# Kernel tuning notes

Measured on AMD Instinct MI355X. Metric: run time of the kernel, lower is better.

## Reference

```python
import jax, jax.numpy as jnp
import numpy as np

B, S, D, H = 2, 2048, 1024, 4
DK = D // H


def setup_inputs() -> dict:
    key = jax.random.key(0)
    ks = jax.random.split(key, 12)
    inp = {
        "Q_input": jax.random.normal(ks[0], (B, S, D), jnp.float32),
        "K": jax.random.normal(ks[1], (B, S, D), jnp.float32),
        "V": jax.random.normal(ks[2], (B, S, D), jnp.float32),
        "T_field": jax.random.normal(ks[3], (32, 32, 16, 16), jnp.float32),
        "Wq_w": jax.random.normal(ks[4], (D, D), jnp.float32) * 0.02,
        "Wq_b": jnp.zeros((D,), jnp.float32),
        "Wo_w": jax.random.normal(ks[5], (D, D), jnp.float32) * 0.02,
        "Wo_b": jnp.zeros((D,), jnp.float32),
        "proj_w": jax.random.normal(ks[6], (24, DK), jnp.float32) * 0.02,
        "proj_b": jnp.zeros((24,), jnp.float32),
        "geo_w": jnp.ones((4,), jnp.float32),
        "temperature": jnp.asarray(1.0, jnp.float32),
    }
    return inp


def _psi(x, proj_w, proj_b):
    # x: (B,H,S,DK) -> 16D real biquaternion via (A,B,Theta) -> A*exp(Th)+B*exp(i*Th)
    gen = x @ proj_w.T + proj_b                      # (B,H,S,24)
    A, Bg = gen[..., 0:8], gen[..., 8:16]
    Th = jnp.clip(gen[..., 16:24], -8.0, 8.0)
    psi_real = A * jnp.exp(Th) + Bg * jnp.cos(Th)
    psi_imag = Bg * jnp.sin(Th)
    return jnp.concatenate([psi_real, psi_imag], axis=-1)  # (B,H,S,16)


def reference(Q_input, K, V, T_field, Wq_w, Wq_b, Wo_w, Wo_b, proj_w, proj_b, geo_w, temperature):
    b, sq, d = Q_input.shape
    sk = K.shape[1]
    dk = d // H
    Q = (Q_input @ Wq_w.T + Wq_b).reshape(b, sq, H, dk).transpose(0, 2, 1, 3)
    Kh = K.reshape(b, sk, H, dk).transpose(0, 2, 1, 3)
    Vh = V.reshape(b, sk, H, dk).transpose(0, 2, 1, 3)
    pq = _psi(Q, proj_w, proj_b)   # (b,H,sq,16)
    pk = _psi(Kh, proj_w, proj_b)  # (b,H,sk,16)
    qr, qi = pq[..., :8], pq[..., 8:]
    kr, ki = pk[..., :8], pk[..., 8:]
    # tensor: real part of complex inner product; spinor: imaginary (rotational) part
    tensor = jnp.einsum('bhqd,bhkd->bhqk', qr, kr) + jnp.einsum('bhqd,bhkd->bhqk', qi, ki)
    spinor = jnp.einsum('bhqd,bhkd->bhqk', qr, ki) - jnp.einsum('bhqd,bhkd->bhqk', qi, kr)
    qn2 = jnp.sum(pq * pq, -1)  # (b,H,sq)
    kn2 = jnp.sum(pk * pk, -1)  # (b,H,sk)
    gram = qn2[..., :, None] * kn2[..., None, :]
    # wedge: antisymmetric span magnitude (Gram residual)
    wedge = jnp.sqrt(jnp.maximum(gram - tensor**2 - spinor**2, 0.0) + 1e-6)
    # hodge: amplitude contraction (rank-2 -> rank-1 conservation)
    hodge = jnp.sqrt(qn2 + 1e-6)[..., :, None] * jnp.sqrt(kn2 + 1e-6)[..., None, :]
    scores = (geo_w[0] * wedge + geo_w[1] * tensor + geo_w[2] * spinor + geo_w[3] * hodge) / 4.0
    scores = scores / temperature
    w = jax.nn.softmax(scores, axis=-1)              # dropout disabled (eval)
    out = jnp.einsum('bhqk,bhkd->bhqd', w, Vh)
    out = out.transpose(0, 2, 1, 3).reshape(b, sq, d)
    return out @ Wo_w.T + Wo_b
```

## Files before the change

### kernel.cpp

```cpp
#include <hip/hip_runtime.h>
#include <hip/hip_bf16.h>
#include <math.h>

#define B_ 2
#define S_ 2048
#define D_ 1024
#define H_ 4
#define DK_ 256
#define NJ 24
#define NG 96
#define KTA 128
#define NT2 (S_ / KTA)

typedef _Float16 f16;
typedef _Float16 f16x2 __attribute__((ext_vector_type(2)));
typedef _Float16 f16x4 __attribute__((ext_vector_type(4)));
typedef _Float16 f16x8 __attribute__((ext_vector_type(8)));
typedef float f32x16 __attribute__((ext_vector_type(16)));
typedef float v2f __attribute__((ext_vector_type(2)));

__global__ __launch_bounds__(256) void k_prep(
    const float* __restrict__ Wq_w, const float* __restrict__ proj_w,
    const float* __restrict__ Wq_b, const float* __restrict__ proj_b,
    const float* __restrict__ Wo_w, const float* __restrict__ V,
    f16* __restrict__ Mf, f16* __restrict__ Mkf,
    float* __restrict__ cbias, float* __restrict__ pbias,
    f16* __restrict__ Wf, f16* __restrict__ Vt2, float* __restrict__ khm) {
  __shared__ f16 tile[64][72];
  const int bid = blockIdx.x;
  const int t = threadIdx.x;
  if (bid < 384) {
    int tid = bid * 256 + t;
    int hj = tid >> 10, d = tid & 1023;
    int h = hj / NJ, j = hj - h * NJ;
    const float* wq = Wq_w + (size_t)(h * DK_) * D_ + d;
    const float* pw = proj_w + j * DK_;
    float acc = 0.f;
#pragma unroll 8
    for (int k = 0; k < DK_; ++k) acc += wq[(size_t)k * D_] * pw[k];
    Mf[(size_t)hj * D_ + d] = (f16)acc;
  } else if (bid == 384) {
    if (t < NG) {
      int h = t / NJ, j = t - h * NJ;
      float acc = proj_b[j];
      for (int k = 0; k < DK_; ++k) acc += Wq_b[h * DK_ + k] * proj_w[j * DK_ + k];
      cbias[t] = acc;
      pbias[t] = proj_b[j];
    }
    if (t < 8) ((unsigned int*)khm)[t] = 0u;
  } else if (bid < 769) {
    int tid = (bid - 385) * 256 + t;
    int hj = tid >> 10, d = tid & 1023;
    int h = hj / NJ, j = hj - h * NJ;
    float v = ((d >> 8) == h) ? proj_w[j * DK_ + (d & 255)] : 0.f;
    Mkf[tid] = (f16)v;
  } else if (bid < 1281) {
    int i = ((bid - 769) * 256 + t) * 8;
    float4 a = *(const float4*)(Wo_w + i);
    float4 b = *(const float4*)(Wo_w + i + 4);
    f16x8 o = {(f16)a.x, (f16)a.y, (f16)a.z, (f16)a.w,
               (f16)b.x, (f16)b.y, (f16)b.z, (f16)b.w};
    *(f16x8*)(Wf + i) = o;
  } else {
    int vbid = bid - 1281;
    int s0 = (vbid & 31) * 64, c0 = ((vbid >> 5) & 3) * 64;
    int bh = vbid >> 7;
    int b = bh >> 2, h = bh & 3;
    const float* src = V + (size_t)b * S_ * D_ + h * DK_ + c0;
#pragma unroll
    for (int u = 0; u < 4; ++u) {
      int row = (t >> 4) + 16 * u;
      int c4 = (t & 15) * 4;
      float4 v = *(const float4*)(src + (size_t)(s0 + row) * D_ + c4);
      tile[c4 + 0][row] = (f16)v.x;
      tile[c4 + 1][row] = (f16)v.y;
      tile[c4 + 2][row] = (f16)v.z;
      tile[c4 + 3][row] = (f16)v.w;
    }
    __syncthreads();
#pragma unroll
    for (int u = 0; u < 2; ++u) {
      int sid = t + 256 * u;
      int sgroup = sid & 7, dkl = sid >> 3;
      int dk = c0 + dkl, s = s0 + sgroup * 8;
      int wv = dk >> 5, qq = dk & 31;
      int kt = s >> 7, ks = (s >> 4) & 7, lhh = (s >> 3) & 1;
      size_t idx = ((((size_t)(bh * 8 + wv) * 16 + kt) * 8 + ks) * 2 + lhh) * 256 + qq * 8;
      *(f16x8*)(Vt2 + idx) = *(const f16x8*)&tile[dkl][sgroup * 8];
    }
  }
}

__global__ __launch_bounds__(256, 1) void k_gen(
    const float* __restrict__ Q, const float* __restrict__ Kin,
    const f16* __restrict__ Mf, const f16* __restrict__ Mkf,
    const float* __restrict__ cbias, const float* __restrict__ pbias,
    f16* __restrict__ pqF, float* __restrict__ qn2,
    f16* __restrict__ pkF, float* __restrict__ kn2,
    float* __restrict__ khm) {
  __shared__ __align__(16) f16 Xs[8192];
  __shared__ __align__(16) f16 Bs[24576];
  __shared__ __align__(16) float redP[4][32][96];
  __shared__ float genL[32][100];

  const int t = threadIdx.x;
  const int w = t >> 6, lane = t & 63;
  const int l31 = lane & 31, lh = lane >> 5;
  const bool isQ = blockIdx.x < 128;
  const int r0 = (isQ ? blockIdx.x : blockIdx.x - 128) * 32;
  const float* X = isQ ? Q : Kin;
  const f16* Bf = isQ ? Mf : Mkf;
  const float* bias = isQ ? cbias : pbias;

  int xrow[8], xk4[8];
#pragma unroll
  for (int u = 0; u < 8; ++u) {
    int idx = t + 256 * u;
    xrow[u] = idx >> 6;
    xk4[u] = idx & 63;
  }
  int bcol[12], bkg[12];
#pragma unroll
  for (int u = 0; u < 12; ++u) {
    int idx = t + 256 * u;
    bcol[u] = idx >> 5;
    bkg[u] = idx & 31;
  }

  float4 xr[8];
  f16x8 br[12];
#define XLOAD(K0)                                                              \
  {                                                                            \
    _Pragma("unroll") for (int u = 0; u < 8; ++u) xr[u] =                      \
        *(const float4*)(X + (size_t)(r0 + xrow[u]) * D_ + (K0) + xk4[u] * 4); \
  }
#define BLOAD(K0)                                                            \
  {                                                                          \
    _Pragma("unroll") for (int u = 0; u < 12; ++u) br[u] =                   \
        *(const f16x8*)(Bf + (size_t)bcol[u] * D_ + (K0) + bkg[u] * 8);      \
  }
#define XWRITE()                                                            \
  {                                                                         \
    _Pragma("unroll") for (int u = 0; u < 8; ++u) {                         \
      f16x4 v = {(f16)xr[u].x, (f16)xr[u].y, (f16)xr[u].z, (f16)xr[u].w};   \
      *(f16x4*)&Xs[((xk4[u] >> 1) * 32 + xrow[u]) * 8 + (xk4[u] & 1) * 4] = v; \
    }                                                                       \
  }
#define BWRITE()                                                            \
  {                                                                         \
    _Pragma("unroll") for (int u = 0; u < 12; ++u)                          \
        *(f16x8*)&Bs[(bcol[u] >> 5) * 8192 + bkg[u] * 256 +                 \
                     (bcol[u] & 31) * 8] = br[u];                           \
  }

  XLOAD(0);
  BLOAD(0);
  XWRITE();
  BWRITE();
  __syncthreads();

  f32x16 acc0{}, acc1{}, acc2{};
  for (int ch = 0; ch < 4; ++ch) {
    if (ch < 3) {
      XLOAD((ch + 1) * 256);
      BLOAD((ch + 1) * 256);
    }
#pragma unroll
    for (int i = 0; i < 4; ++i) {
      const int kk = w * 4 + i;
      const int off = (kk * 2 + lh) * 256 + l31 * 8;
      f16x8 af = *(const f16x8*)&Xs[off];
      f16x8 b0 = *(const f16x8*)&Bs[off];
      f16x8 b1 = *(const f16x8*)&Bs[8192 + off];
      f16x8 b2 = *(const f16x8*)&Bs[16384 + off];
      acc0 = __builtin_amdgcn_mfma_f32_32x32x16_f16(af, b0, acc0, 0, 0, 0);
      acc1 = __builtin_amdgcn_mfma_f32_32x32x16_f16(af, b1, acc1, 0, 0, 0);
      acc2 = __builtin_amdgcn_mfma_f32_32x32x16_f16(af, b2, acc2, 0, 0, 0);
    }
    __syncthreads();
    if (ch < 3) {
      XWRITE();
      BWRITE();
      __syncthreads();
    }
  }
#undef XLOAD
#undef BLOAD
#undef XWRITE
#undef BWRITE

#pragma unroll
  for (int r = 0; r < 16; ++r) {
    const int row = (r & 3) + 8 * (r >> 2) + 4 * lh;
    redP[w][row][l31] = acc0[r];
    redP[w][row][32 + l31] = acc1[r];
    redP[w][row][64 + l31] = acc2[r];
  }
  __syncthreads();

  {
    const int row = t >> 3, cg = t & 7;
#pragma unroll
    for (int c = 0; c < 12; ++c) {
      int col = cg * 12 + c;
      genL[row][col] = redP[0][row][col] + redP[1][row][col] +
                       redP[2][row][col] + redP[3][row][col] + bias[col];
    }
  }
  __syncthreads();

  {
    const int rg = t >> 6;
    const int hh = (t & 63) >> 4;
    const int ii = t & 15;
    const int j = ii & 7;
    f16* po = isQ ? pqF : pkF;
    float* n2o = isQ ? qn2 : kn2;
    float mx = 0.f;
#pragma unroll 2
    for (int r = 0; r < 8; ++r) {
      int row = rg * 8 + r;
      int g = r0 + row;
      int b = g >> 11, s = g & (S_ - 1);
      const float* gl = &genL[row][hh * NJ];
      float A = gl[j], Bg = gl[8 + j];
      float Th = fminf(fmaxf(gl[16 + j], -8.f), 8.f);
      float val = (ii < 8) ? (A * __expf(Th) + Bg * __cosf(Th)) : (Bg * __sinf(Th));
      size_t base = (size_t)(b * H_ + hh) * S_ + s;
      po[base * 16 + ii] = (f16)val;
      float sq = val * val;
#pragma unroll
      for (int off = 1; off < 16; off <<= 1) sq += __shfl_xor(sq, off);
      if (ii == 0) {
        n2o[base] = sq;
        mx = fmaxf(mx, sq);
      }
    }
    if (!isQ && ii == 0) {
      int g = r0;
      int b = g >> 11;
      atomicMax((unsigned int*)&khm[b * H_ + hh], __float_as_uint(mx));
    }
  }
}

__global__ __launch_bounds__(512, 4) void k_attn(
    const f16* __restrict__ pqF, const float* __restrict__ qn2,
    const f16* __restrict__ pkF, const float* __restrict__ kn2,
    const f16* __restrict__ Vt2, const float* __restrict__ geo_w,
    const float* __restrict__ temp, const float* __restrict__ khm,
    f16* __restrict__ attnF) {
  __shared__ __align__(16) float kn2s[2][KTA];
  __shared__ __align__(16) float khs[2][KTA];
  __shared__ float sPart[8][32];
  __shared__ float linvL[32];
  __shared__ __align__(16) f16 Plds[2][16][32][8];

  const int t = threadIdx.x;
  const int w = t >> 6;
  const int lane = t & 63;
  const int q_ = lane & 31;
  const int lh = lane >> 5;

  const int bid = blockIdx.x;
  const int bh = bid & 7, qt = bid >> 3;
  const int q0 = qt * 32;
  const int b = bh >> 2, h = bh & 3;

  const size_t bhS = (size_t)bh * S_;
  const f16* pkb = pkF + bhS * 16;
  const float* kn2b = kn2 + bhS;

  const float scale = 0.25f / temp[0] * 1.4426950408889634f;
  const float g0s = geo_w[0] * scale, g1s = geo_w[1] * scale, g2s = geo_w[2] * scale;
  const float g3s = geo_w[3] * scale;

  const f16x8 bq = *(const f16x8*)(pqF + (bhS + q0 + q_) * 16 + lh * 8);
  const float qn2q = qn2[bhS + q0 + q_];
  const float qh = sqrtf(qn2q + 1e-6f);
  const float qh3 = qh * g3s;
  const float sumg = fabsf(g0s) + fabsf(g1s) + fabsf(g2s) + fabsf(g3s);
  const float Mhat = sumg * qh * sqrtf(khm[bh] + 1e-6f) - 4.328085123f;

  const v2f qn2v = {qn2q, qn2q};
  const v2f g0v = {g0s, g0s}, g1v = {g1s, g1s}, g2v = {g2s, g2s};
  const v2f zero2 = {0.f, 0.f}, eps2 = {1e-6f, 1e-6f};
  const v2f mhv = {Mhat, Mhat};

  const f16* ap_base = pkb + (size_t)(w * 16 + (q_ & 15)) * 16 +
                       ((q_ < 16) ? lh * 8 : (1 - lh) * 8);
  const f16* vb_lane = Vt2 + (size_t)(bh * 8 + w) * 16 * 4096 + lh * 256 + q_ * 8;

  if (t < KTA) {
    float kv = kn2b[t];
    kn2s[0][t] = kv;
    khs[0][t] = __builtin_amdgcn_sqrtf(kv + 1e-6f);
  }
  float lreg = 0.f;
  f32x16 acc{};
  const f32x16 zacc{};

  f16x8 af = *(const f16x8*)ap_base;
  f16x8 bv[8];
#pragma unroll
  for (int ks = 0; ks < 8; ++ks) bv[ks] = *(const f16x8*)(vb_lane + ks * 512);
  __syncthreads();

  for (int ktl = 0; ktl < NT2; ++ktl) {
    const int k0l = ktl * KTA;
    const int cb = ktl & 1, nb = cb ^ 1;

    float knv = 0.f;
    if (t < KTA && ktl + 1 < NT2) knv = kn2b[k0l + KTA + t];

    f16x8 afx = af;
    if (q_ >= 16 && lh == 1) afx = -afx;
    __builtin_amdgcn_s_setprio(1);
    f32x16 sc = __builtin_amdgcn_mfma_f32_32x32x16_f16(afx, bq, zacc, 0, 0, 0);
    __builtin_amdgcn_s_setprio(0);
    if (ktl + 1 < NT2) af = *(const f16x8*)(ap_base + (size_t)(k0l + KTA) * 16);

    float pv[8];
    v2f psv = {0.f, 0.f};
#pragma unroll
    for (int rp = 0; rp < 4; ++rp) {
      const int r = 2 * rp;
      const int kb2 = w * 16 + 4 * lh + (rp & 1) * 2 + (rp >> 1) * 8;
      v2f tn = {sc[r], sc[r + 1]};
      v2f sp = {sc[r + 8], sc[r + 9]};
      v2f kn2p = *(const v2f*)&kn2s[cb][kb2];
      v2f khp = *(const v2f*)&khs[cb][kb2];
      v2f wr = qn2v * kn2p - tn * tn - sp * sp;
      wr = __builtin_elementwise_max(wr, zero2) + eps2;
      v2f wg = {__builtin_amdgcn_sqrtf(wr.x), __builtin_amdgcn_sqrtf(wr.y)};
      v2f sv2 = g0v * wg + g1v * tn + g2v * sp + qh3 * khp - mhv;
      v2f p2 = {__builtin_amdgcn_exp2f(sv2.x), __builtin_amdgcn_exp2f(sv2.y)};
      pv[r] = p2.x;
      pv[r + 1] = p2.y;
      psv += p2;
    }
    lreg += psv.x + psv.y;

    if (t < KTA && ktl + 1 < NT2) {
      kn2s[nb][t] = knv;
      khs[nb][t] = __builtin_amdgcn_sqrtf(knv + 1e-6f);
    }
    {
      f16x2 p01 = {(f16)pv[0], (f16)pv[1]};
      f16x2 p23 = {(f16)pv[2], (f16)pv[3]};
      f16x2 p45 = {(f16)pv[4], (f16)pv[5]};
      f16x2 p67 = {(f16)pv[6], (f16)pv[7]};
      *(f16x2*)&Plds[cb][2 * w + 0][q_][4 * lh + 0] = p01;
      *(f16x2*)&Plds[cb][2 * w + 0][q_][4 * lh + 2] = p23;
      *(f16x2*)&Plds[cb][2 * w + 1][q_][4 * lh + 0] = p45;
      *(f16x2*)&Plds[cb][2 * w + 1][q_][4 * lh + 2] = p67;
    }
    __syncthreads();

    __builtin_amdgcn_s_setprio(1);
#pragma unroll
    for (int ks = 0; ks < 8; ++ks) {
      f16x8 pa = *(const f16x8*)&Plds[cb][2 * ks + lh][q_][0];
      acc = __builtin_amdgcn_mfma_f32_32x32x16_f16(pa, bv[ks], acc, 0, 0, 0);
    }
    __builtin_amdgcn_s_setprio(0);
    if (ktl + 1 < NT2) {
      const f16* vbn = vb_lane + (size_t)(ktl + 1) * 4096;
#pragma unroll
      for (int ks = 0; ks < 8; ++ks) bv[ks] = *(const f16x8*)(vbn + ks * 512);
    }
  }

  lreg += __shfl_xor(lreg, 32);
  if (lh == 0) sPart[w][q_] = lreg;
  __syncthreads();
  if (t < 32) {
    float s8 = 0.f;
#pragma unroll
    for (int i = 0; i < 8; ++i) s8 += sPart[i][t];
    linvL[t] = 1.f / s8;
  }
  __syncthreads();
  const size_t obase = ((size_t)b * S_ + q0) * D_ + h * DK_ + w * 32 + q_;
#pragma unroll
  for (int r = 0; r < 16; ++r) {
    const int row = (r & 3) + 8 * (r >> 2) + 4 * lh;
    attnF[obase + (size_t)row * D_] = (f16)(acc[r] * linvL[row]);
  }
}

__global__ __launch_bounds__(256, 1) void k_wo(const f16* __restrict__ A,
                                               const f16* __restrict__ Wt,
                                               const float* __restrict__ bias,
                                               float* __restrict__ C) {
  __shared__ __align__(16) f16 Abuf[2][128 * 64];
  __shared__ __align__(16) f16 Bbuf[2][128 * 64];
  const int t = threadIdx.x;
  const int w = t >> 6, lane = t & 63;
  const int wr = w >> 1, wc = w & 1;
  const int brow = blockIdx.y * 128, bcol = blockIdx.x * 128;

  int srow[4], skof[4];
#pragma unroll
  for (int u = 0; u < 4; ++u) {
    int c = t + 256 * u;
    int sub = c >> 6, l6 = c & 63;
    srow[u] = (sub >> 2) * 32 + (l6 & 31);
    skof[u] = (sub & 3) * 16 + (l6 >> 5) * 8;
  }

  uint4 ra0, ra1, ra2, ra3, rb0, rb1, rb2, rb3;
#define LOAD_TILE(K0)                                                        \
  {                                                                          \
    ra0 = *(const uint4*)(A + (size_t)(brow + srow[0]) * D_ + (K0) + skof[0]); \
    ra1 = *(const uint4*)(A + (size_t)(brow + srow[1]) * D_ + (K0) + skof[1]); \
    ra2 = *(const uint4*)(A + (size_t)(brow + srow[2]) * D_ + (K0) + skof[2]); \
    ra3 = *(const uint4*)(A + (size_t)(brow + srow[3]) * D_ + (K0) + skof[3]); \
    rb0 = *(const uint4*)(Wt + (size_t)(bcol + srow[0]) * D_ + (K0) + skof[0]); \
    rb1 = *(const uint4*)(Wt + (size_t)(bcol + srow[1]) * D_ + (K0) + skof[1]); \
    rb2 = *(const uint4*)(Wt + (size_t)(bcol + srow[2]) * D_ + (K0) + skof[2]); \
    rb3 = *(const uint4*)(Wt + (size_t)(bcol + srow[3]) * D_ + (K0) + skof[3]); \
  }
#define WRITE_TILE(BUF)                                       \
  {                                                           \
    *(uint4*)&Abuf[BUF][(t + 0) * 8] = ra0;                   \
    *(uint4*)&Abuf[BUF][(t + 256) * 8] = ra1;                 \
    *(uint4*)&Abuf[BUF][(t + 512) * 8] = ra2;                 \
    *(uint4*)&Abuf[BUF][(t + 768) * 8] = ra3;                 \
    *(uint4*)&Bbuf[BUF][(t + 0) * 8] = rb0;                   \
    *(uint4*)&Bbuf[BUF][(t + 256) * 8] = rb1;                 \
    *(uint4*)&Bbuf[BUF][(t + 512) * 8] = rb2;                 \
    *(uint4*)&Bbuf[BUF][(t + 768) * 8] = rb3;                 \
  }

  f32x16 acc00{}, acc01{}, acc10{}, acc11{};

  LOAD_TILE(0);
  WRITE_TILE(0);
  LOAD_TILE(64);
  __syncthreads();

  int cur = 0;
  for (int kt = 0; kt < 16; ++kt) {
    const int am0 = (wr * 2 + 0) * 4, am1 = (wr * 2 + 1) * 4;
    const int bn0 = (wc * 2 + 0) * 4, bn1 = (wc * 2 + 1) * 4;
#pragma unroll
    for (int kk = 0; kk < 4; ++kk) {
      f16x8 a0 = *(const f16x8*)&Abuf[cur][(am0 + kk) * 512 + lane * 8];
      f16x8 a1 = *(const f16x8*)&Abuf[cur][(am1 + kk) * 512 + lane * 8];
      f16x8 b0 = *(const f16x8*)&Bbuf[cur][(bn0 + kk) * 512 + lane * 8];
      f16x8 b1 = *(const f16x8*)&Bbuf[cur][(bn1 + kk) * 512 + lane * 8];
      acc00 = __builtin_amdgcn_mfma_f32_32x32x16_f16(a0, b0, acc00, 0, 0, 0);
      acc01 = __builtin_amdgcn_mfma_f32_32x32x16_f16(a0, b1, acc01, 0, 0, 0);
      acc10 = __builtin_amdgcn_mfma_f32_32x32x16_f16(a1, b0, acc10, 0, 0, 0);
      acc11 = __builtin_amdgcn_mfma_f32_32x32x16_f16(a1, b1, acc11, 0, 0, 0);
    }
    if (kt + 1 < 16) {
      WRITE_TILE(cur ^ 1);
      if (kt + 2 < 16) LOAD_TILE((kt + 2) * 64);
    }
    __syncthreads();
    cur ^= 1;
  }

  const int l31 = lane & 31, lh = lane >> 5;
  const float bv0 = bias[bcol + (wc * 2 + 0) * 32 + l31];
  const float bv1 = bias[bcol + (wc * 2 + 1) * 32 + l31];
#pragma unroll
  for (int r = 0; r < 16; ++r) {
    const int row = (r & 3) + 8 * (r >> 2) + 4 * lh;
    const size_t m0r = (size_t)(brow + (wr * 2 + 0) * 32 + row) * D_;
    const size_t m1r = (size_t)(brow + (wr * 2 + 1) * 32 + row) * D_;
    C[m0r + bcol + (wc * 2 + 0) * 32 + l31] = acc00[r] + bv0;
    C[m0r + bcol + (wc * 2 + 1) * 32 + l31] = acc01[r] + bv1;
    C[m1r + bcol + (wc * 2 + 0) * 32 + l31] = acc10[r] + bv0;
    C[m1r + bcol + (wc * 2 + 1) * 32 + l31] = acc11[r] + bv1;
  }
#undef LOAD_TILE
#undef WRITE_TILE
}

extern "C" void kernel_launch(void* const* d_in, const int* in_sizes, int n_in,
                              void* d_out, int out_size, void* d_ws, size_t ws_size,
                              hipStream_t stream) {
  const float* Q_input = (const float*)d_in[0];
  const float* K = (const float*)d_in[1];
  const float* V = (const float*)d_in[2];
  const float* Wq_w = (const float*)d_in[4];
  const float* Wq_b = (const float*)d_in[5];
  const float* Wo_w = (const float*)d_in[6];
  const float* Wo_b = (const float*)d_in[7];
  const float* proj_w = (const float*)d_in[8];
  const float* proj_b = (const float*)d_in[9];
  const float* geo_w = (const float*)d_in[10];
  const float* temp = (const float*)d_in[11];

  float* ws = (float*)d_ws;
  float* cbias = ws;
  float* pbias = cbias + 128;
  float* khm = pbias + 128;
  f16* Mf = (f16*)(khm + 128);
  f16* Mkf = Mf + 98304;
  float* qn2 = (float*)(Mkf + 98304);
  float* kn2 = qn2 + 16384;
  f16* pqF = (f16*)(kn2 + 16384);
  f16* pkF = pqF + 262144;
  f16* Vt2 = pkF + 262144;
  f16* attnF = Vt2 + 4194304;
  f16* Wf = attnF + 4194304;
  float* out = (float*)d_out;

  k_prep<<<dim3(2305), dim3(256), 0, stream>>>(Wq_w, proj_w, Wq_b, proj_b, Wo_w,
                                               V, Mf, Mkf, cbias, pbias, Wf, Vt2,
                                               khm);
  k_gen<<<dim3(256), dim3(256), 0, stream>>>(Q_input, K, Mf, Mkf, cbias, pbias,
                                             pqF, qn2, pkF, kn2, khm);
  k_attn<<<dim3(512), dim3(512), 0, stream>>>(pqF, qn2, pkF, kn2, Vt2, geo_w,
                                              temp, khm, attnF);
  k_wo<<<dim3(8, 32), dim3(256), 0, stream>>>(attnF, Wf, Wo_b, out);
}
```

Measured before the change: 103.0 us.

## Double attention key tile to 256 per iteration, halving barriers

The attention loop now processes 256 keys per iteration instead of 128. Each wave issues two score MFMAs and two sets of softmax exponentials, and sixteen PV MFMAs per step, with the shared score buffer and norm buffers doubled. The intent is to halve the per-tile barrier and loop overhead and expose more independent MFMA work. The cost is higher register and LDS use, and launch bounds are relaxed from four to two blocks per CU, which lowers occupancy.

```diff
diff --git a/kernel.cpp b/kernel.cpp
--- a/kernel.cpp
+++ b/kernel.cpp
@@ -9,8 +9,8 @@
 #define DK_ 256
 #define NJ 24
 #define NG 96
-#define KTA 128
-#define NT2 (S_ / KTA)
+#define KT2 256
+#define NT256 (S_ / KT2)
 
 typedef _Float16 f16;
 typedef _Float16 f16x2 __attribute__((ext_vector_type(2)));
@@ -244,17 +244,17 @@
   }
 }
 
-__global__ __launch_bounds__(512, 4) void k_attn(
+__global__ __launch_bounds__(512, 2) void k_attn(
     const f16* __restrict__ pqF, const float* __restrict__ qn2,
     const f16* __restrict__ pkF, const float* __restrict__ kn2,
     const f16* __restrict__ Vt2, const float* __restrict__ geo_w,
     const float* __restrict__ temp, const float* __restrict__ khm,
     f16* __restrict__ attnF) {
-  __shared__ __align__(16) float kn2s[2][KTA];
-  __shared__ __align__(16) float khs[2][KTA];
+  __shared__ __align__(16) float kn2s[2][KT2];
+  __shared__ __align__(16) float khs[2][KT2];
   __shared__ float sPart[8][32];
   __shared__ float linvL[32];
-  __shared__ __align__(16) f16 Plds[2][16][32][8];
+  __shared__ __align__(16) f16 Plds[2][32][32][8];
 
   const int t = threadIdx.x;
   const int w = t >> 6;
@@ -287,11 +287,11 @@
   const v2f zero2 = {0.f, 0.f}, eps2 = {1e-6f, 1e-6f};
   const v2f mhv = {Mhat, Mhat};
 
-  const f16* ap_base = pkb + (size_t)(w * 16 + (q_ & 15)) * 16 +
+  const f16* ap_base = pkb + (size_t)(w * 32 + (q_ & 15)) * 16 +
                        ((q_ < 16) ? lh * 8 : (1 - lh) * 8);
-  const f16* vb_lane = Vt2 + (size_t)(bh * 8 + w) * 16 * 4096 + lh * 256 + q_ * 8;
-
-  if (t < KTA) {
+  const f16* vt_base = Vt2 + (size_t)(bh * 8 + w) * 16 * 4096 + lh * 256 + q_ * 8;
+
+  if (t < KT2) {
     float kv = kn2b[t];
     kn2s[0][t] = kv;
     khs[0][t] = __builtin_amdgcn_sqrtf(kv + 1e-6f);
@@ -300,34 +300,40 @@
   f32x16 acc{};
   const f32x16 zacc{};
 
-  f16x8 af = *(const f16x8*)ap_base;
-  f16x8 bv[8];
-#pragma unroll
-  for (int ks = 0; ks < 8; ++ks) bv[ks] = *(const f16x8*)(vb_lane + ks * 512);
-  __syncthreads();
-
-  for (int ktl = 0; ktl < NT2; ++ktl) {
-    const int k0l = ktl * KTA;
+  f16x8 af0 = *(const f16x8*)ap_base;
+  f16x8 af1 = *(const f16x8*)(ap_base + 256);
+  f16x8 bv[8], bvB[8];
+#pragma unroll
+  for (int ks = 0; ks < 8; ++ks) bv[ks] = *(const f16x8*)(vt_base + ks * 512);
+#pragma unroll
+  for (int ks = 0; ks < 8; ++ks) bvB[ks] = *(const f16x8*)(vt_base + 4096 + ks * 512);
+  __syncthreads();
+
+  for (int ktl = 0; ktl < NT256; ++ktl) {
     const int cb = ktl & 1, nb = cb ^ 1;
 
     float knv = 0.f;
-    if (t < KTA && ktl + 1 < NT2) knv = kn2b[k0l + KTA + t];
-
-    f16x8 afx = af;
-    if (q_ >= 16 && lh == 1) afx = -afx;
+    if (t < KT2 && ktl + 1 < NT256) knv = kn2b[ktl * KT2 + KT2 + t];
+
+    f16x8 a0 = af0, a1 = af1;
+    if (q_ >= 16 && lh == 1) { a0 = -a0; a1 = -a1; }
     __builtin_amdgcn_s_setprio(1);
-    f32x16 sc = __builtin_amdgcn_mfma_f32_32x32x16_f16(afx, bq, zacc, 0, 0, 0);
+    f32x16 sc0 = __builtin_amdgcn_mfma_f32_32x32x16_f16(a0, bq, zacc, 0, 0, 0);
+    f32x16 sc1 = __builtin_amdgcn_mfma_f32_32x32x16_f16(a1, bq, zacc, 0, 0, 0);
     __builtin_amdgcn_s_setprio(0);
-    if (ktl + 1 < NT2) af = *(const f16x8*)(ap_base + (size_t)(k0l + KTA) * 16);
-
-    float pv[8];
+    if (ktl + 1 < NT256) {
+      af0 = *(const f16x8*)(ap_base + (size_t)(ktl + 1) * 4096);
+      af1 = *(const f16x8*)(ap_base + (size_t)(ktl + 1) * 4096 + 256);
+    }
+
+    float pv0[8], pv1[8];
     v2f psv = {0.f, 0.f};
 #pragma unroll
     for (int rp = 0; rp < 4; ++rp) {
       const int r = 2 * rp;
-      const int kb2 = w * 16 + 4 * lh + (rp & 1) * 2 + (rp >> 1) * 8;
-      v2f tn = {sc[r], sc[r + 1]};
-      v2f sp = {sc[r + 8], sc[r + 9]};
+      const int kb2 = w * 32 + 4 * lh + (rp & 1) * 2 + (rp >> 1) * 8;
+      v2f tn = {sc0[r], sc0[r + 1]};
+      v2f sp = {sc0[r + 8], sc0[r + 9]};
       v2f kn2p = *(const v2f*)&kn2s[cb][kb2];
       v2f khp = *(const v2f*)&khs[cb][kb2];
       v2f wr = qn2v * kn2p - tn * tn - sp * sp;
@@ -335,25 +341,50 @@
       v2f wg = {__builtin_amdgcn_sqrtf(wr.x), __builtin_amdgcn_sqrtf(wr.y)};
       v2f sv2 = g0v * wg + g1v * tn + g2v * sp + qh3 * khp - mhv;
       v2f p2 = {__builtin_amdgcn_exp2f(sv2.x), __builtin_amdgcn_exp2f(sv2.y)};
-      pv[r] = p2.x;
-      pv[r + 1] = p2.y;
+      pv0[r] = p2.x;
+      pv0[r + 1] = p2.y;
       psv += p2;
     }
+#pragma unroll
+    for (int rp = 0; rp < 4; ++rp) {
+      const int r = 2 * rp;
+      const int kb2 = w * 32 + 16 + 4 * lh + (rp & 1) * 2 + (rp >> 1) * 8;
+      v2f tn = {sc1[r], sc1[r + 1]};
+      v2f sp = {sc1[r + 8], sc1[r + 9]};
+      v2f kn2p = *(const v2f*)&kn2s[cb][kb2];
+      v2f khp = *(const v2f*)&khs[cb][kb2];
+      v2f wr = qn2v * kn2p - tn * tn - sp * sp;
+      wr = __builtin_elementwise_max(wr, zero2) + eps2;
+      v2f wg = {__builtin_amdgcn_sqrtf(wr.x), __builtin_amdgcn_sqrtf(wr.y)};
+      v2f sv2 = g0v * wg + g1v * tn + g2v * sp + qh3 * khp - mhv;
+      v2f p2 = {__builtin_amdgcn_exp2f(sv2.x), __builtin_amdgcn_exp2f(sv2.y)};
+      pv1[r] = p2.x;
+      pv1[r + 1] = p2.y;
+      psv += p2;
+    }
     lreg += psv.x + psv.y;
 
-    if (t < KTA && ktl + 1 < NT2) {
+    if (t < KT2 && ktl + 1 < NT256) {
       kn2s[nb][t] = knv;
       khs[nb][t] = __builtin_amdgcn_sqrtf(knv + 1e-6f);
     }
     {
-      f16x2 p01 = {(f16)pv[0], (f16)pv[1]};
-      f16x2 p23 = {(f16)pv[2], (f16)pv[3]};
-      f16x2 p45 = {(f16)pv[4], (f16)pv[5]};
-      f16x2 p67 = {(f16)pv[6], (f16)pv[7]};
-      *(f16x2*)&Plds[cb][2 * w + 0][q_][4 * lh + 0] = p01;
-      *(f16x2*)&Plds[cb][2 * w + 0][q_][4 * lh + 2] = p23;
-      *(f16x2*)&Plds[cb][2 * w + 1][q_][4 * lh + 0] = p45;
-      *(f16x2*)&Plds[cb][2 * w + 1][q_][4 * lh + 2] = p67;
+      f16x2 a01 = {(f16)pv0[0], (f16)pv0[1]};
+      f16x2 a23 = {(f16)pv0[2], (f16)pv0[3]};
+      f16x2 a45 = {(f16)pv0[4], (f16)pv0[5]};
+      f16x2 a67 = {(f16)pv0[6], (f16)pv0[7]};
+      *(f16x2*)&Plds[cb][4 * w + 0][q_][4 * lh + 0] = a01;
+      *(f16x2*)&Plds[cb][4 * w + 0][q_][4 * lh + 2] = a23;
+      *(f16x2*)&Plds[cb][4 * w + 1][q_][4 * lh + 0] = a45;
+      *(f16x2*)&Plds[cb][4 * w + 1][q_][4 * lh + 2] = a67;
+      f16x2 b01 = {(f16)pv1[0], (f16)pv1[1]};
+      f16x2 b23 = {(f16)pv1[2], (f16)pv1[3]};
+      f16x2 b45 = {(f16)pv1[4], (f16)pv1[5]};
+      f16x2 b67 = {(f16)pv1[6], (f16)pv1[7]};
+      *(f16x2*)&Plds[cb][4 * w + 2][q_][4 * lh + 0] = b01;
+      *(f16x2*)&Plds[cb][4 * w + 2][q_][4 * lh + 2] = b23;
+      *(f16x2*)&Plds[cb][4 * w + 3][q_][4 * lh + 0] = b45;
+      *(f16x2*)&Plds[cb][4 * w + 3][q_][4 * lh + 2] = b67;
     }
     __syncthreads();
 
@@ -363,11 +394,18 @@
       f16x8 pa = *(const f16x8*)&Plds[cb][2 * ks + lh][q_][0];
       acc = __builtin_amdgcn_mfma_f32_32x32x16_f16(pa, bv[ks], acc, 0, 0, 0);
     }
+#pragma unroll
+    for (int ks = 8; ks < 16; ++ks) {
+      f16x8 pa = *(const f16x8*)&Plds[cb][2 * ks + lh][q_][0];
+      acc = __builtin_amdgcn_mfma_f32_32x32x16_f16(pa, bvB[ks - 8], acc, 0, 0, 0);
+    }
     __builtin_amdgcn_s_setprio(0);
-    if (ktl + 1 < NT2) {
-      const f16* vbn = vb_lane + (size_t)(ktl + 1) * 4096;
+    if (ktl + 1 < NT256) {
+      const f16* vbn = vt_base + (size_t)(ktl + 1) * 8192;
 #pragma unroll
       for (int ks = 0; ks < 8; ++ks) bv[ks] = *(const f16x8*)(vbn + ks * 512);
+#pragma unroll
+      for (int ks = 0; ks < 8; ++ks) bvB[ks] = *(const f16x8*)(vbn + 4096 + ks * 512);
     }
   }
 
```

Result: slower. 106.4 us (+3.3%).
